# Performance work log

Hardware: AMD Instinct MI355X
Metric: run time of the kernel (lower is better)

## Reference

```python
import jax, jax.numpy as jnp
import numpy as np

K, S, P = 3, 2, 2  # kernel_size, stride, padding (dilation=1)


def _unfold(xp, k, s, oh, ow):
    """Extract k*k strided patches from a padded array.

    xp: (..., Hp, Wp) -> (..., k*k, oh, ow), window-position ordering (kh, kw)
    matching torch.nn.Unfold (channel-major handled by caller).
    """
    return jnp.stack(
        [xp[..., i:i + s * (oh - 1) + 1:s, j:j + s * (ow - 1) + 1:s]
         for i in range(K) for j in range(K)],
        axis=-3,
    )


def setup_inputs() -> dict:
    key = jax.random.key(0)
    x = jax.random.normal(key, (8, 256, 128, 128), dtype=jnp.float32)
    return {"x": x}


def reference(x):
    b, c, h, w = x.shape
    oh = (h - K + 2 * P) // S + 1
    ow = (w - K + 2 * P) // S + 1

    # channel-wise L2 norm, computed BEFORE unfolding (padding contributes 0 either way)
    n = jnp.sqrt(jnp.sum(x * x, axis=1))            # (b, h, w)
    n_pad = jnp.pad(n, ((0, 0), (P, P), (P, P)))
    n_patch = _unfold(n_pad, K, S, oh, ow)          # (b, k*k, oh, ow)
    # weighting_fn = softmax over the k*k window positions (torch dim=1 of unfolded norm)
    wts = jax.nn.softmax(n_patch, axis=1)           # (b, k*k, oh, ow)

    x_pad = jnp.pad(x, ((0, 0), (0, 0), (P, P), (P, P)))
    x_patch = _unfold(x_pad, K, S, oh, ow)          # (b, c, k*k, oh, ow)

    # weighted sum over window positions
    return jnp.sum(wts[:, None] * x_patch, axis=2)  # (b, c, oh, ow)
```

## Files before the change

### kernel.cpp

```cpp
#include <hip/hip_runtime.h>
#include <math.h>

#define BATCH 8
#define CH    256
#define H     128
#define W     128
#define HW    (H * W)
#define OH    65
#define OW    65
#define NPIX  (OH * OW)
#define CGRP  32

__global__ __launch_bounds__(256) void norm_kernel(const float4* __restrict__ x4,
                                                   float4* __restrict__ n4) {
    __shared__ float4 part[4][64];
    const int lane = threadIdx.x & 63;
    const int wv   = threadIdx.x >> 6;
    const int q    = blockIdx.x * 64 + lane;
    const int b    = (q * 4) >> 14;
    const int qin  = q - b * (HW / 4);

    const float4* p = x4 + (size_t)(b * CH + wv * 64) * (HW / 4) + qin;
    float4 acc = {0.f, 0.f, 0.f, 0.f};
    #pragma unroll 8
    for (int c = 0; c < 64; ++c) {
        float4 v = p[(size_t)c * (HW / 4)];
        acc.x += v.x * v.x; acc.y += v.y * v.y;
        acc.z += v.z * v.z; acc.w += v.w * v.w;
    }
    part[wv][lane] = acc;
    __syncthreads();
    if (wv == 0) {
        float4 a0 = part[0][lane], a1 = part[1][lane];
        float4 a2 = part[2][lane], a3 = part[3][lane];
        float4 r;
        r.x = sqrtf(a0.x + a1.x + a2.x + a3.x);
        r.y = sqrtf(a0.y + a1.y + a2.y + a3.y);
        r.z = sqrtf(a0.z + a1.z + a2.z + a3.z);
        r.w = sqrtf(a0.w + a1.w + a2.w + a3.w);
        n4[q] = r;
    }
}

__global__ __launch_bounds__(256) void pool_kernel(const float* __restrict__ x,
                                                   const float* __restrict__ n,
                                                   float* __restrict__ out) {
    int p = blockIdx.x * blockDim.x + threadIdx.x;
    if (p >= NPIX) return;
    const int b  = blockIdx.y;
    const int cg = blockIdx.z;
    const int oh = p / OW;
    const int ow = p - oh * OW;
    const int iw0 = ow * 2 - 2;

    const float* nb = n + b * HW;

    float nv[9];
    bool  val[9];
    float m = 0.0f;
    #pragma unroll
    for (int kh = 0; kh < 3; ++kh) {
        int ih = oh * 2 + kh - 2;
        bool vh = (unsigned)ih < (unsigned)H;
        #pragma unroll
        for (int kw = 0; kw < 3; ++kw) {
            int iw = iw0 + kw;
            int k = kh * 3 + kw;
            bool v = vh && ((unsigned)iw < (unsigned)W);
            val[k] = v;
            nv[k]  = v ? nb[ih * W + iw] : 0.0f;
            m = fmaxf(m, nv[k]);
        }
    }
    float denom = 0.0f;
    float wts[9];
    #pragma unroll
    for (int k = 0; k < 9; ++k) {
        float e = __expf(nv[k] - m);
        denom += e;
        wts[k] = val[k] ? e : 0.0f;
    }
    float inv = 1.0f / denom;
    #pragma unroll
    for (int k = 0; k < 9; ++k) wts[k] *= inv;

    int off2[3], offs[3];
    const int iwa = iw0 < 0 ? 0 : iw0;
    const int iwc = (iw0 + 2) > (W - 1) ? (W - 1) : (iw0 + 2);
    #pragma unroll
    for (int r = 0; r < 3; ++r) {
        int ih = oh * 2 + r - 2;
        int ihc = ih < 0 ? 0 : (ih > H - 1 ? H - 1 : ih);
        off2[r] = ihc * W + iwa;
        offs[r] = ihc * W + iwc;
    }

    const float* xb = x + (size_t)(b * CH + cg * CGRP) * HW;
    float*       ob = out + (size_t)(b * CH + cg * CGRP) * NPIX + p;

    #pragma unroll 4
    for (int c = 0; c < CGRP; ++c) {
        const float* xc = xb + (size_t)c * HW;
        float acc = 0.f;
        #pragma unroll
        for (int r = 0; r < 3; ++r) {
            float2 v2 = *(const float2*)(xc + off2[r]);
            float  vs = xc[offs[r]];
            acc += wts[r * 3 + 0] * v2.x + wts[r * 3 + 1] * v2.y + wts[r * 3 + 2] * vs;
        }
        ob[(size_t)c * NPIX] = acc;
    }
}

extern "C" void kernel_launch(void* const* d_in, const int* in_sizes, int n_in,
                              void* d_out, int out_size, void* d_ws, size_t ws_size,
                              hipStream_t stream) {
    const float* x = (const float*)d_in[0];
    float* out = (float*)d_out;
    float* nbuf = (float*)d_ws;

    norm_kernel<<<512, 256, 0, stream>>>((const float4*)x, (float4*)nbuf);

    dim3 grid((NPIX + 255) / 256, BATCH, CH / CGRP);
    pool_kernel<<<grid, 256, 0, stream>>>(x, nbuf, out);
}
```

Baseline: 231.0 us.

## Restructure pool kernel to one output row per block with wave-shuffle window sharing

```diff
diff --git a/kernel.cpp b/kernel.cpp
--- a/kernel.cpp
+++ b/kernel.cpp
@@ -9,7 +9,8 @@
 #define OH    65
 #define OW    65
 #define NPIX  (OH * OW)
-#define CGRP  32
+#define CSPLIT 4
+#define CPW   (CH / CSPLIT / 4)
 
 __global__ __launch_bounds__(256) void norm_kernel(const float4* __restrict__ x4,
                                                    float4* __restrict__ n4) {
@@ -45,70 +46,88 @@
 __global__ __launch_bounds__(256) void pool_kernel(const float* __restrict__ x,
                                                    const float* __restrict__ n,
                                                    float* __restrict__ out) {
-    int p = blockIdx.x * blockDim.x + threadIdx.x;
-    if (p >= NPIX) return;
+    __shared__ float wts[OW][9];
+    const int oh = blockIdx.x;
     const int b  = blockIdx.y;
-    const int cg = blockIdx.z;
-    const int oh = p / OW;
-    const int ow = p - oh * OW;
-    const int iw0 = ow * 2 - 2;
+    const int z  = blockIdx.z;
+    const int t  = threadIdx.x;
 
-    const float* nb = n + b * HW;
+    if (t < OW) {
+        const float* nb = n + b * HW;
+        const int iw0 = 2 * t - 2;
+        float ww[9];
+        bool  vl[9];
+        float m = 0.f;
+        #pragma unroll
+        for (int r = 0; r < 3; ++r) {
+            int ih = 2 * oh + r - 2;
+            bool vh = (unsigned)ih < (unsigned)H;
+            int ihc = ih < 0 ? 0 : (ih > H - 1 ? H - 1 : ih);
+            #pragma unroll
+            for (int kw = 0; kw < 3; ++kw) {
+                int iw = iw0 + kw;
+                bool v = vh && ((unsigned)iw < (unsigned)W);
+                int iwc = iw < 0 ? 0 : (iw > W - 1 ? W - 1 : iw);
+                float nv = v ? nb[ihc * W + iwc] : 0.f;
+                vl[r * 3 + kw] = v;
+                ww[r * 3 + kw] = nv;
+                m = fmaxf(m, nv);
+            }
+        }
+        float d = 0.f;
+        #pragma unroll
+        for (int k = 0; k < 9; ++k) {
+            float e = __expf(ww[k] - m);
+            d += e;
+            ww[k] = vl[k] ? e : 0.f;
+        }
+        float inv = 1.f / d;
+        #pragma unroll
+        for (int k = 0; k < 9; ++k) wts[t][k] = ww[k] * inv;
+    }
+    __syncthreads();
 
-    float nv[9];
-    bool  val[9];
-    float m = 0.0f;
+    const int lane = t & 63;
+    const int wv   = t >> 6;
+
+    float w0[9], w64[9];
     #pragma unroll
-    for (int kh = 0; kh < 3; ++kh) {
-        int ih = oh * 2 + kh - 2;
-        bool vh = (unsigned)ih < (unsigned)H;
-        #pragma unroll
-        for (int kw = 0; kw < 3; ++kw) {
-            int iw = iw0 + kw;
-            int k = kh * 3 + kw;
-            bool v = vh && ((unsigned)iw < (unsigned)W);
-            val[k] = v;
-            nv[k]  = v ? nb[ih * W + iw] : 0.0f;
-            m = fmaxf(m, nv[k]);
-        }
-    }
-    float denom = 0.0f;
-    float wts[9];
-    #pragma unroll
-    for (int k = 0; k < 9; ++k) {
-        float e = __expf(nv[k] - m);
-        denom += e;
-        wts[k] = val[k] ? e : 0.0f;
-    }
-    float inv = 1.0f / denom;
-    #pragma unroll
-    for (int k = 0; k < 9; ++k) wts[k] *= inv;
+    for (int k = 0; k < 9; ++k) { w0[k] = wts[lane][k]; w64[k] = wts[OW - 1][k]; }
 
-    int off2[3], offs[3];
-    const int iwa = iw0 < 0 ? 0 : iw0;
-    const int iwc = (iw0 + 2) > (W - 1) ? (W - 1) : (iw0 + 2);
+    int rb[3];
     #pragma unroll
     for (int r = 0; r < 3; ++r) {
-        int ih = oh * 2 + r - 2;
+        int ih = 2 * oh + r - 2;
         int ihc = ih < 0 ? 0 : (ih > H - 1 ? H - 1 : ih);
-        off2[r] = ihc * W + iwa;
-        offs[r] = ihc * W + iwc;
+        rb[r] = ihc * W;
     }
 
-    const float* xb = x + (size_t)(b * CH + cg * CGRP) * HW;
-    float*       ob = out + (size_t)(b * CH + cg * CGRP) * NPIX + p;
+    const int cbase = z * (CH / CSPLIT) + wv * CPW;
+    const float* xb = x + (size_t)(b * CH + cbase) * HW;
+    float*       ob = out + (size_t)(b * CH + cbase) * NPIX + oh * OW;
 
     #pragma unroll 4
-    for (int c = 0; c < CGRP; ++c) {
+    for (int c = 0; c < CPW; ++c) {
         const float* xc = xb + (size_t)c * HW;
-        float acc = 0.f;
+        float2 own[3], prev[3];
+        #pragma unroll
+        for (int r = 0; r < 3; ++r)
+            own[r] = *(const float2*)(xc + rb[r] + 2 * lane);
         #pragma unroll
         for (int r = 0; r < 3; ++r) {
-            float2 v2 = *(const float2*)(xc + off2[r]);
-            float  vs = xc[offs[r]];
-            acc += wts[r * 3 + 0] * v2.x + wts[r * 3 + 1] * v2.y + wts[r * 3 + 2] * vs;
+            prev[r].x = __shfl_up(own[r].x, 1);
+            prev[r].y = __shfl_up(own[r].y, 1);
         }
-        ob[(size_t)c * NPIX] = acc;
+        float a0 = 0.f, a1 = 0.f;
+        #pragma unroll
+        for (int r = 0; r < 3; ++r) {
+            a0 += w0[r * 3 + 0] * prev[r].x + w0[r * 3 + 1] * prev[r].y
+                + w0[r * 3 + 2] * own[r].x;
+            a1 += w64[r * 3 + 0] * own[r].x + w64[r * 3 + 1] * own[r].y;
+        }
+        float* oc = ob + (size_t)c * NPIX;
+        oc[lane] = a0;
+        if (lane == 63) oc[OW - 1] = a1;
     }
 }
 
@@ -121,6 +140,6 @@
 
     norm_kernel<<<512, 256, 0, stream>>>((const float4*)x, (float4*)nbuf);
 
-    dim3 grid((NPIX + 255) / 256, BATCH, CH / CGRP);
+    dim3 grid(OH, BATCH, CSPLIT);
     pool_kernel<<<grid, 256, 0, stream>>>(x, nbuf, out);
 }
```

New measurement: 239.7 us. 1.04x slower.
